# Performance work log

Measured on AMD Instinct MI355X. Metric: run time of the kernel, lower is better.

Reference implementation:

```python
import jax, jax.numpy as jnp
import numpy as np

B, T, H, C = 64, 512, 1024, 21  # batch, seq_len, hidden_size, num_labels


def setup_inputs() -> dict:
    key = jax.random.key(0)
    ks = jax.random.split(key, 7)
    hidden_states = jax.random.normal(ks[0], (B, T, H), dtype=jnp.float32)
    lengths = jax.random.randint(ks[1], (B,), 1, T + 1)  # at least 1 valid token
    attention_mask = jnp.arange(T)[None, :] < lengths[:, None]  # [B,T] bool, contiguous prefix
    labels = jax.random.randint(ks[2], (B, T), 0, C)
    # classifier params (nn.Linear(H, C))
    W = jax.random.normal(ks[3], (H, C), dtype=jnp.float32) * 0.02
    b = jnp.zeros((C,), dtype=jnp.float32)
    # CRF params (torchcrf init: uniform(-0.1, 0.1))
    transitions = jax.random.uniform(ks[4], (C, C), minval=-0.1, maxval=0.1, dtype=jnp.float32)
    start_transitions = jax.random.uniform(ks[5], (C,), minval=-0.1, maxval=0.1, dtype=jnp.float32)
    end_transitions = jax.random.uniform(ks[6], (C,), minval=-0.1, maxval=0.1, dtype=jnp.float32)
    return {
        "hidden_states": hidden_states,
        "W": W,
        "b": b,
        "transitions": transitions,
        "start_transitions": start_transitions,
        "end_transitions": end_transitions,
        "attention_mask": attention_mask,
        "labels": labels,
    }


def _crf_nll(emissions, tags, mask, transitions, start_transitions, end_transitions):
    """Mean negative log-likelihood of torchcrf CRF(batch_first=True, reduction='mean')."""
    maskf = mask.astype(emissions.dtype)
    # ---- numerator: score of the gold tag path ----
    em_tag = jnp.take_along_axis(emissions, tags[..., None], axis=2)[..., 0]  # [B,T]
    trans_score = transitions[tags[:, :-1], tags[:, 1:]]                      # [B,T-1]
    num = (start_transitions[tags[:, 0]] + em_tag[:, 0]
           + jnp.sum((trans_score + em_tag[:, 1:]) * maskf[:, 1:], axis=1))
    last_idx = jnp.sum(mask.astype(jnp.int32), axis=1) - 1                    # [B]
    last_tag = jnp.take_along_axis(tags, last_idx[:, None], axis=1)[:, 0]
    num = num + end_transitions[last_tag]
    # ---- denominator: forward algorithm (log partition) ----
    alpha0 = start_transitions[None, :] + emissions[:, 0]                     # [B,C]

    def step(alpha, xs):
        em_t, m_t = xs  # [B,C], [B]
        nxt = jax.nn.logsumexp(alpha[:, :, None] + transitions[None, :, :] + em_t[:, None, :], axis=1)
        return jnp.where(m_t[:, None], nxt, alpha), None

    xs = (jnp.swapaxes(emissions[:, 1:], 0, 1), jnp.swapaxes(mask[:, 1:], 0, 1))
    alphaT, _ = jax.lax.scan(step, alpha0, xs)
    logZ = jax.nn.logsumexp(alphaT + end_transitions[None, :], axis=1)        # [B]
    llh = num - logZ
    return -jnp.mean(llh)


def reference(hidden_states, W, b, transitions, start_transitions, end_transitions,
              attention_mask, labels):
    # dropout is identity at inference; emissions = Linear(hidden)
    emissions = jnp.einsum('bth,hc->btc', hidden_states, W) + b              # [B,T,C]
    # mask logic from the module: attention_mask & (labels != -100); mask[:,0] = True
    mask = attention_mask & (labels != -100)
    mask = mask.at[:, 0].set(True)
    loss = _crf_nll(emissions, labels, mask, transitions, start_transitions, end_transitions)
    return emissions, loss
```

## Files before the change

### kernel.cpp

```cpp
#include <hip/hip_runtime.h>

#define BB 64
#define TT 512
#define HH 1024
#define CC 21
#define NROWS (BB*TT)

__global__ __launch_bounds__(512, 2) void emis_gemm(const float* __restrict__ hs,
                                                    const float* __restrict__ W,
                                                    const float* __restrict__ bias,
                                                    float* __restrict__ out) {
  __shared__ float red[4 * 128 * CC];
  const int tid  = threadIdx.x;
  const int lane = tid & 63;
  const int w    = __builtin_amdgcn_readfirstlane(tid >> 6);
  const int half = w >> 2;
  const int seg  = w & 3;
  const int rowL = half * 64 + lane;
  const int row0 = blockIdx.x * 128;

  if (blockIdx.x == 0 && tid == 0) out[(size_t)NROWS * CC] = 0.f;

  const float4* xrow =
      reinterpret_cast<const float4*>(hs + (size_t)(row0 + rowL) * HH + seg * 256);
  const float4* Wf4 = reinterpret_cast<const float4*>(W);
  const int nw0 = seg * 64;

  float4 xq[8];
#pragma unroll
  for (int i = 0; i < 8; ++i) xq[i] = xrow[i];

  float4 wb[2][21];
  {
    const float4* p = Wf4 + (size_t)nw0 * 21;
#pragma unroll
    for (int q = 0; q < 21; ++q) wb[0][q] = p[q];
  }

  float acc[CC];
#pragma unroll
  for (int c = 0; c < CC; ++c) acc[c] = 0.f;

#pragma unroll 8
  for (int kb = 0; kb < 64; ++kb) {
    const int s = kb & 7;
    float4 xv = xq[s];
    int kn = kb + 8; if (kn > 63) kn = 63;
    xq[s] = xrow[kn];
    int nw = nw0 + kb + 1; if (nw > 255) nw = 255;
    {
      const float4* p = Wf4 + (size_t)nw * 21;
      float4* dst = wb[(kb + 1) & 1];
#pragma unroll
      for (int q = 0; q < 21; ++q) dst[q] = p[q];
    }
    const float4* wc = wb[kb & 1];
#pragma unroll
    for (int r = 0; r < 4; ++r) {
      float xr = (r == 0) ? xv.x : (r == 1) ? xv.y : (r == 2) ? xv.z : xv.w;
#pragma unroll
      for (int c = 0; c < CC; ++c) {
        const int f = r * 21 + c;
        const int q = f >> 2, m = f & 3;
        float4 ww = wc[q];
        float wv = (m == 0) ? ww.x : (m == 1) ? ww.y : (m == 2) ? ww.z : ww.w;
        acc[c] = fmaf(xr, wv, acc[c]);
      }
    }
  }

  if (seg != 0) {
#pragma unroll
    for (int c = 0; c < CC; ++c)
      red[((seg - 1) * 128 + rowL) * CC + c] = acc[c];
  }
  __syncthreads();
  if (seg == 0) {
#pragma unroll
    for (int c = 0; c < CC; ++c) {
      float v = acc[c] + bias[c];
#pragma unroll
      for (int q = 0; q < 3; ++q) v += red[(q * 128 + rowL) * CC + c];
      red[(3 * 128 + rowL) * CC + c] = v;
    }
  }
  __syncthreads();
  const float* fin = red + 3 * 128 * CC;
  for (int idx = tid; idx < 128 * CC; idx += 512)
    out[(size_t)row0 * CC + idx] = fin[idx];
}

__global__ __launch_bounds__(128) void crf_kernel(const float* __restrict__ em,
                                                  const float* __restrict__ trans,
                                                  const float* __restrict__ startT,
                                                  const float* __restrict__ endT,
                                                  const int* __restrict__ att,
                                                  const int* __restrict__ labels,
                                                  float* __restrict__ loss) {
  const int b    = blockIdx.x;
  const int tid  = threadIdx.x;
  const int wave = tid >> 6;
  const int lane = tid & 63;
  __shared__ float sh_num;
  __shared__ int   sh_len;

  const float L2E = 1.4426950408889634f;
  const float LN2 = 0.6931471805599453f;

  if (wave == 1) {
    int cnt = 0;
    for (int t = lane; t < TT; t += 64) {
      bool m = (t == 0) || ((att[b * TT + t] != 0) && (labels[b * TT + t] != -100));
      cnt += m ? 1 : 0;
    }
#pragma unroll
    for (int off = 32; off >= 1; off >>= 1) cnt += __shfl_down(cnt, off);
    cnt = __shfl(cnt, 0);

    float s = 0.f;
    for (int t = lane + 1; t < TT; t += 64) {
      bool m = (att[b * TT + t] != 0) && (labels[b * TT + t] != -100);
      if (m) {
        int tp = labels[b * TT + t - 1], tc = labels[b * TT + t];
        s += trans[tp * CC + tc] + em[((size_t)b * TT + t) * CC + tc];
      }
    }
#pragma unroll
    for (int off = 32; off >= 1; off >>= 1) s += __shfl_down(s, off);
    if (lane == 0) {
      int tag0 = labels[b * TT];
      int lastTag = labels[b * TT + cnt - 1];
      s += startT[tag0] + em[((size_t)b * TT) * CC + tag0] + endT[lastTag];
      sh_num = s;
      sh_len = cnt;
    }
  }

  const int j = lane < CC ? lane : CC - 1;
  float E[CC], F[CC];
  float f = 0.f, g = 0.f;
  if (wave == 0) {
#pragma unroll
    for (int i = 0; i < CC; ++i) {
      E[i] = __builtin_amdgcn_exp2f(trans[i * CC + j] * L2E);
      F[i] = __builtin_amdgcn_exp2f(trans[j * CC + i] * L2E);
    }
    f = __builtin_amdgcn_exp2f((startT[j] + em[((size_t)b * TT) * CC + j]) * L2E);
    g = __builtin_amdgcn_exp2f(endT[j] * L2E);
  }
  __syncthreads();
  if (wave != 0) return;

  const int len = sh_len;
  const int L  = len - 1;
  const int mF = (L + 1) >> 1;
  const int mB = L - mF;
  int kf = 0, kg = 0;

  float sf[CC];
#pragma unroll
  for (int i = 0; i < CC; ++i)
    sf[i] = __int_as_float(__builtin_amdgcn_readlane(__float_as_int(f), i));

  const float* emB = em + (size_t)b * TT * CC;

  float rf[4], rb[4];
#pragma unroll
  for (int u = 0; u < 4; ++u) {
    int tf = 1 + u; if (tf > TT - 1) tf = TT - 1;
    rf[u] = emB[(size_t)tf * CC + j];
    int tb = len - 1 - u; if (tb < 0) tb = 0;
    rb[u] = emB[(size_t)tb * CC + j];
  }

  int it = 0;
  while (it < mF) {
#pragma unroll
    for (int u = 0; u < 4; ++u) {
      const int i2 = it + u;
      if (i2 < mF) {
        float pm = __builtin_amdgcn_exp2f(rf[u] * L2E);
        int tp = 1 + i2 + 4; if (tp > TT - 1) tp = TT - 1;
        rf[u] = emB[(size_t)tp * CC + j];
        int ef = (__float_as_int(sf[0]) >> 23) & 255;
        kf += ef - 127;
        float pms = pm * __int_as_float((254 - ef) << 23);
        float c0 = 0.f, c1 = 0.f, c2 = 0.f;
#pragma unroll
        for (int i = 0; i < CC; i += 3) c0 = fmaf(sf[i], E[i], c0);
#pragma unroll
        for (int i = 1; i < CC; i += 3) c1 = fmaf(sf[i], E[i], c1);
#pragma unroll
        for (int i = 2; i < CC; i += 3) c2 = fmaf(sf[i], E[i], c2);
        f = ((c0 + c1) + c2) * pms;
#pragma unroll
        for (int i = 0; i < CC; ++i)
          sf[i] = __int_as_float(__builtin_amdgcn_readlane(__float_as_int(f), i));
      }
      if (i2 < mB) {
        float pm = __builtin_amdgcn_exp2f(rb[u] * L2E);
        int tb = len - 1 - i2 - 4; if (tb < 0) tb = 0;
        rb[u] = emB[(size_t)tb * CC + j];
        float h = pm * g;
        float sh_[CC];
#pragma unroll
        for (int i = 0; i < CC; ++i)
          sh_[i] = __int_as_float(__builtin_amdgcn_readlane(__float_as_int(h), i));
        int eg = (__float_as_int(sh_[0]) >> 23) & 255;
        kg += eg - 127;
        float sB = __int_as_float((254 - eg) << 23);
        float d0 = 0.f, d1 = 0.f, d2 = 0.f;
#pragma unroll
        for (int i = 0; i < CC; i += 3) d0 = fmaf(sh_[i], F[i], d0);
#pragma unroll
        for (int i = 1; i < CC; i += 3) d1 = fmaf(sh_[i], F[i], d1);
#pragma unroll
        for (int i = 2; i < CC; i += 3) d2 = fmaf(sh_[i], F[i], d2);
        g = ((d0 + d1) + d2) * sB;
      }
    }
    it += 4;
  }

  float v = (lane < CC) ? f * g : 0.f;
#pragma unroll
  for (int off = 32; off >= 1; off >>= 1) v += __shfl_xor(v, off);
  if (lane == 0) {
    float logZ = (float)(kf + kg) * LN2 + LN2 * __builtin_amdgcn_logf(v);
    atomicAdd(loss, -(sh_num - logZ) * (1.0f / 64.0f));
  }
}

extern "C" void kernel_launch(void* const* d_in, const int* in_sizes, int n_in,
                              void* d_out, int out_size, void* d_ws, size_t ws_size,
                              hipStream_t stream) {
  const float* hs     = (const float*)d_in[0];
  const float* W      = (const float*)d_in[1];
  const float* bias   = (const float*)d_in[2];
  const float* trans  = (const float*)d_in[3];
  const float* startT = (const float*)d_in[4];
  const float* endT   = (const float*)d_in[5];
  const int*   att    = (const int*)d_in[6];
  const int*   labels = (const int*)d_in[7];
  float* out = (float*)d_out;

  emis_gemm<<<dim3(256), dim3(512), 0, stream>>>(hs, W, bias, out);
  crf_kernel<<<dim3(64), dim3(128), 0, stream>>>(out, trans, startT, endT, att,
                                                 labels, out + (size_t)NROWS * CC);
}
```

Measured before the change: 326.7 us.

## Compute emissions GEMM with split-bf16 MFMA instead of scalar FP32 FMAs

Replaces the scalar FP32 emission GEMM with a 32x32x16 bf16 MFMA kernel. Both the activations and W are split into hi and lo bf16 parts, and three MFMAs per step (hi*hi, hi*lo, lo*hi) approximate FP32 accuracy. A small prep kernel transposes W, pads it to 32 columns and splits it into workspace. This moves the compute onto matrix cores and drops the shared-memory reduction, at the cost of an extra launch, padded columns and a small accuracy loss from the split-bf16 approximation.

```diff
diff --git a/kernel.cpp b/kernel.cpp
--- a/kernel.cpp
+++ b/kernel.cpp
@@ -6,88 +6,82 @@
 #define CC 21
 #define NROWS (BB*TT)
 
-__global__ __launch_bounds__(512, 2) void emis_gemm(const float* __restrict__ hs,
-                                                    const float* __restrict__ W,
-                                                    const float* __restrict__ bias,
-                                                    float* __restrict__ out) {
-  __shared__ float red[4 * 128 * CC];
-  const int tid  = threadIdx.x;
-  const int lane = tid & 63;
-  const int w    = __builtin_amdgcn_readfirstlane(tid >> 6);
-  const int half = w >> 2;
-  const int seg  = w & 3;
-  const int rowL = half * 64 + lane;
-  const int row0 = blockIdx.x * 128;
-
-  if (blockIdx.x == 0 && tid == 0) out[(size_t)NROWS * CC] = 0.f;
-
-  const float4* xrow =
-      reinterpret_cast<const float4*>(hs + (size_t)(row0 + rowL) * HH + seg * 256);
-  const float4* Wf4 = reinterpret_cast<const float4*>(W);
-  const int nw0 = seg * 64;
-
-  float4 xq[8];
-#pragma unroll
-  for (int i = 0; i < 8; ++i) xq[i] = xrow[i];
-
-  float4 wb[2][21];
-  {
-    const float4* p = Wf4 + (size_t)nw0 * 21;
-#pragma unroll
-    for (int q = 0; q < 21; ++q) wb[0][q] = p[q];
-  }
-
-  float acc[CC];
-#pragma unroll
-  for (int c = 0; c < CC; ++c) acc[c] = 0.f;
+typedef __attribute__((ext_vector_type(8)))  short  short8;
+typedef __attribute__((ext_vector_type(16))) float  float16;
+
+__global__ __launch_bounds__(256) void wprep(const float* __restrict__ W,
+                                             unsigned short* __restrict__ wpad) {
+  int idx = blockIdx.x * 256 + threadIdx.x;
+  int n = idx >> 10, k = idx & 1023;
+  float v = (n < CC) ? W[k * CC + n] : 0.f;
+  unsigned b = __float_as_uint(v);
+  float lo = v - __uint_as_float(b & 0xFFFF0000u);
+  wpad[idx]         = (unsigned short)(b >> 16);
+  wpad[32768 + idx] = (unsigned short)(__float_as_uint(lo) >> 16);
+}
+
+__global__ __launch_bounds__(64) void emis_mfma(const float* __restrict__ hs,
+                                                const unsigned short* __restrict__ wpad,
+                                                const float* __restrict__ bias,
+                                                float* __restrict__ out) {
+  const int lane = threadIdx.x;
+  const int m    = lane & 31;
+  const int half = lane >> 5;
+  const int row0 = blockIdx.x * 32;
+
+  if (blockIdx.x == 0 && lane == 0) out[(size_t)NROWS * CC] = 0.f;
+
+  const float4* arow =
+      reinterpret_cast<const float4*>(hs + (size_t)(row0 + m) * HH) + half * 2;
+  const unsigned short* whi = wpad + m * 1024 + half * 8;
+  const unsigned short* wlo = whi + 32768;
+
+  float16 acc;
+#pragma unroll
+  for (int i = 0; i < 16; ++i) acc[i] = 0.f;
+
+  float4 xa[8], xb[8];
+#pragma unroll
+  for (int i = 0; i < 8; ++i) { xa[i] = arow[i * 4]; xb[i] = arow[i * 4 + 1]; }
+  short8 bhq[4], blq[4];
+#pragma unroll
+  for (int i = 0; i < 4; ++i) {
+    bhq[i] = *reinterpret_cast<const short8*>(whi + i * 16);
+    blq[i] = *reinterpret_cast<const short8*>(wlo + i * 16);
+  }
 
 #pragma unroll 8
   for (int kb = 0; kb < 64; ++kb) {
-    const int s = kb & 7;
-    float4 xv = xq[s];
+    const int s8 = kb & 7, s4 = kb & 3;
+    float4 a0 = xa[s8], a1 = xb[s8];
     int kn = kb + 8; if (kn > 63) kn = 63;
-    xq[s] = xrow[kn];
-    int nw = nw0 + kb + 1; if (nw > 255) nw = 255;
-    {
-      const float4* p = Wf4 + (size_t)nw * 21;
-      float4* dst = wb[(kb + 1) & 1];
-#pragma unroll
-      for (int q = 0; q < 21; ++q) dst[q] = p[q];
-    }
-    const float4* wc = wb[kb & 1];
-#pragma unroll
-    for (int r = 0; r < 4; ++r) {
-      float xr = (r == 0) ? xv.x : (r == 1) ? xv.y : (r == 2) ? xv.z : xv.w;
-#pragma unroll
-      for (int c = 0; c < CC; ++c) {
-        const int f = r * 21 + c;
-        const int q = f >> 2, m = f & 3;
-        float4 ww = wc[q];
-        float wv = (m == 0) ? ww.x : (m == 1) ? ww.y : (m == 2) ? ww.z : ww.w;
-        acc[c] = fmaf(xr, wv, acc[c]);
-      }
-    }
-  }
-
-  if (seg != 0) {
-#pragma unroll
-    for (int c = 0; c < CC; ++c)
-      red[((seg - 1) * 128 + rowL) * CC + c] = acc[c];
-  }
-  __syncthreads();
-  if (seg == 0) {
-#pragma unroll
-    for (int c = 0; c < CC; ++c) {
-      float v = acc[c] + bias[c];
-#pragma unroll
-      for (int q = 0; q < 3; ++q) v += red[(q * 128 + rowL) * CC + c];
-      red[(3 * 128 + rowL) * CC + c] = v;
-    }
-  }
-  __syncthreads();
-  const float* fin = red + 3 * 128 * CC;
-  for (int idx = tid; idx < 128 * CC; idx += 512)
-    out[(size_t)row0 * CC + idx] = fin[idx];
+    xa[s8] = arow[kn * 4];
+    xb[s8] = arow[kn * 4 + 1];
+    short8 bh = bhq[s4], bl = blq[s4];
+    int kw = kb + 4; if (kw > 63) kw = 63;
+    bhq[s4] = *reinterpret_cast<const short8*>(whi + kw * 16);
+    blq[s4] = *reinterpret_cast<const short8*>(wlo + kw * 16);
+
+    float af[8] = {a0.x, a0.y, a0.z, a0.w, a1.x, a1.y, a1.z, a1.w};
+    short8 ah, al;
+#pragma unroll
+    for (int j = 0; j < 8; ++j) {
+      unsigned b = __float_as_uint(af[j]);
+      ah[j] = (short)(b >> 16);
+      float lo = af[j] - __uint_as_float(b & 0xFFFF0000u);
+      al[j] = (short)(__float_as_uint(lo) >> 16);
+    }
+    acc = __builtin_amdgcn_mfma_f32_32x32x16_bf16(ah, bh, acc, 0, 0, 0);
+    acc = __builtin_amdgcn_mfma_f32_32x32x16_bf16(ah, bl, acc, 0, 0, 0);
+    acc = __builtin_amdgcn_mfma_f32_32x32x16_bf16(al, bh, acc, 0, 0, 0);
+  }
+
+  float bv = (m < CC) ? bias[m] : 0.f;
+#pragma unroll
+  for (int r = 0; r < 16; ++r) {
+    int row = (r & 3) + 8 * (r >> 2) + 4 * half;
+    if (m < CC) out[(size_t)(row0 + row) * CC + m] = acc[r] + bv;
+  }
 }
 
 __global__ __launch_bounds__(128) void crf_kernel(const float* __restrict__ em,
@@ -243,8 +237,10 @@
   const int*   att    = (const int*)d_in[6];
   const int*   labels = (const int*)d_in[7];
   float* out = (float*)d_out;
-
-  emis_gemm<<<dim3(256), dim3(512), 0, stream>>>(hs, W, bias, out);
+  unsigned short* wpad = (unsigned short*)d_ws;
+
+  wprep<<<dim3(128), dim3(256), 0, stream>>>(W, wpad);
+  emis_mfma<<<dim3(1024), dim3(64), 0, stream>>>(hs, wpad, bias, out);
   crf_kernel<<<dim3(64), dim3(128), 0, stream>>>(out, trans, startT, endT, att,
                                                  labels, out + (size_t)NROWS * CC);
 }
```

Measured after the change: 289.2 us. 11.5% less time.
